# Optimization experiments

Measured on AMD Instinct MI355X. Metric: run time of the kernel, lower is better.

Reference implementation:

```python
import jax, jax.numpy as jnp
import numpy as np
import math

B, H, N, D = 4, 16, 2048, 64
EPS = 1e-8


def setup_inputs() -> dict:
    key = jax.random.key(0)
    kq, kk, kv = jax.random.split(key, 3)
    Q = jax.random.normal(kq, (B, H, N, D), dtype=jnp.float32)
    K = jax.random.normal(kk, (B, H, N, D), dtype=jnp.float32)
    V = jax.random.normal(kv, (B, H, N, D), dtype=jnp.float32)
    # learnable per-head scale, init g0 = log2(N^2 - N)
    g0 = math.log2(N * N - N)
    qk_scale = jnp.full((H,), g0, dtype=jnp.float32)
    # causal mask, broadcast over (B, H)
    M = jnp.tril(jnp.ones((N, N), dtype=bool))
    return {"Q": Q, "K": K, "V": V, "qk_scale": qk_scale, "M": M}


def reference(Q, K, V, qk_scale, M):
    # L2-normalize Q and K along head dim (cosine attention)
    Q_hat = Q / (jnp.sqrt(jnp.sum(Q * Q, axis=-1, keepdims=True)) + EPS)
    K_hat = K / (jnp.sqrt(jnp.sum(K * K, axis=-1, keepdims=True)) + EPS)
    g = qk_scale[None, :, None, None]  # per-head learnable temperature
    scores = jnp.einsum('bhnd,bhmd->bhnm', Q_hat * g, K_hat)
    scores = jnp.where(M, scores, -jnp.inf)
    attn = jax.nn.softmax(scores, axis=-1)  # stable max-subtract softmax
    return jnp.einsum('bhnm,bhmd->bhnd', attn, V)
```

## Files before the change

### kernel.cpp

```cpp
#include <hip/hip_runtime.h>


#define BATCH 4
#define HEADS 16
#define SEQ   2048
#define DIM   64
#define EPS   1e-8f
#define LOG2E 1.44269504088896340736f

typedef short bf16x8 __attribute__((ext_vector_type(8)));
typedef short s16x4  __attribute__((ext_vector_type(4)));
typedef float fx16   __attribute__((ext_vector_type(16)));
typedef unsigned int u32x4 __attribute__((ext_vector_type(4)));

static __device__ __forceinline__ short f2bf(float x) {
    unsigned u = __float_as_uint(x);
    unsigned r = (u + 0x7fffu + ((u >> 16) & 1u)) >> 16;
    return (short)r;
}
static __device__ __forceinline__ unsigned cvt_pk(float lo, float hi) {
    unsigned r;
    asm("v_cvt_pk_bf16_f32 %0, %1, %2" : "=v"(r) : "v"(lo), "v"(hi));
    return r;
}
static __device__ __forceinline__ void gload_lds16(const short* g, short* l) {
    __builtin_amdgcn_global_load_lds(
        (const __attribute__((address_space(1))) void*)g,
        (__attribute__((address_space(3))) void*)l, 16, 0, 0);
}

__global__ __launch_bounds__(256) void norm_k(
    const float* __restrict__ K, short* __restrict__ Kn)
{
    const int tid  = threadIdx.x;
    const int lane = tid & 63;
    long long rid = (long long)blockIdx.x * 16 + (tid >> 6) * 4 + (lane >> 4);
    const int c4 = (lane & 15) * 4;

    const float* src = K + rid * DIM;
    float4 v = *(const float4*)(src + c4);
    float ss = v.x * v.x + v.y * v.y + v.z * v.z + v.w * v.w;
    ss += __shfl_xor(ss, 1);
    ss += __shfl_xor(ss, 2);
    ss += __shfl_xor(ss, 4);
    ss += __shfl_xor(ss, 8);
    float s = 1.0f / (sqrtf(ss) + EPS);

    const int bh = (int)(rid >> 11);
    const int n  = (int)(rid & 2047);
    const int kt = n >> 6;
    const int r  = n & 63;
    short* dst = Kn + ((size_t)bh << 17) + (kt << 12) + (r << 6);

    s16x4 o;
    o[0] = f2bf(v.x * s);
    o[1] = f2bf(v.y * s);
    o[2] = f2bf(v.z * s);
    o[3] = f2bf(v.w * s);
    *(s16x4*)(dst + (c4 ^ ((r & 7) << 3))) = o;
}

#define TLDS 68

__global__ __launch_bounds__(256) void transpose_v(
    const float* __restrict__ V, short* __restrict__ Vt)
{
    const int nt = blockIdx.x;
    const int bh = blockIdx.y;
    const float* Vb = V + ((size_t)bh * SEQ + (size_t)nt * 64) * DIM;
    short* Vo = Vt + ((size_t)bh << 17) + (nt << 12);

    __shared__ short lds[DIM * TLDS];
    const int t  = threadIdx.x;
    const int cg = t & 15;
    const int rr = t >> 4;

#pragma unroll
    for (int i = 0; i < 4; ++i) {
        int n  = rr + i * 16;
        int d0 = cg * 4;
        float4 v = *(const float4*)(Vb + (size_t)n * DIM + d0);
        lds[(d0 + 0) * TLDS + n] = f2bf(v.x);
        lds[(d0 + 1) * TLDS + n] = f2bf(v.y);
        lds[(d0 + 2) * TLDS + n] = f2bf(v.z);
        lds[(d0 + 3) * TLDS + n] = f2bf(v.w);
    }
    __syncthreads();
#pragma unroll
    for (int i = 0; i < 4; ++i) {
        int d  = rr + i * 16;
        int nl = cg * 4;
        s16x4 o;
        o[0] = lds[d * TLDS + nl + 0];
        o[1] = lds[d * TLDS + nl + 1];
        o[2] = lds[d * TLDS + nl + 2];
        o[3] = lds[d * TLDS + nl + 3];
        *(s16x4*)(Vo + (d << 6) + (nl ^ ((d & 7) << 3))) = o;
    }
}

__global__ __launch_bounds__(128) void attn_fwd(
    const float* __restrict__ Q, const float* __restrict__ scale,
    const short* __restrict__ Kn, const short* __restrict__ Vt,
    float* __restrict__ out)
{
    const int lid = blockIdx.x;
    const int bh  = (lid & 7) * 8 + ((lid >> 3) & 7);
    const int qt  = 31 - (lid >> 6);
    const int tid = threadIdx.x;
    const int w   = tid >> 6;
    const int l   = tid & 63;
    const int lq  = l & 31;
    const int hi  = l >> 5;

    const int wlo  = qt * 64 + w * 32;
    const int qrow = wlo + lq;

    const short* Kb = Kn + ((size_t)bh << 17);
    const short* Vb = Vt + ((size_t)bh << 17);

    __shared__ __align__(16) short ldsK[2][64 * 64];
    __shared__ __align__(16) short ldsV[2][64 * 64];

    const int toff = tid * 8;

#pragma unroll
    for (int s = 0; s < 4; ++s) {
        gload_lds16(Kb + s * 1024 + toff, &ldsK[0][s * 1024 + toff]);
        gload_lds16(Vb + s * 1024 + toff, &ldsV[0][s * 1024 + toff]);
    }

    const float* Qrow = Q + ((size_t)bh * SEQ + qrow) * DIM;
    float qv[4][8];
    float ss = 0.f;
#pragma unroll
    for (int c = 0; c < 4; ++c) {
        float4 a = *(const float4*)(Qrow + c * 16 + hi * 8);
        float4 b = *(const float4*)(Qrow + c * 16 + hi * 8 + 4);
        qv[c][0] = a.x; qv[c][1] = a.y; qv[c][2] = a.z; qv[c][3] = a.w;
        qv[c][4] = b.x; qv[c][5] = b.y; qv[c][6] = b.z; qv[c][7] = b.w;
#pragma unroll
        for (int jj = 0; jj < 8; ++jj) ss += qv[c][jj] * qv[c][jj];
    }
    ss += __shfl_xor(ss, 32);
    const float g  = scale[bh & (HEADS - 1)];
    const float sc = g * LOG2E / (sqrtf(ss) + EPS);

    bf16x8 qb[4];
#pragma unroll
    for (int c = 0; c < 4; ++c) {
        u32x4 wds;
#pragma unroll
        for (int m = 0; m < 4; ++m)
            wds[m] = cvt_pk(qv[c][2 * m] * sc, qv[c][2 * m + 1] * sc);
        qb[c] = __builtin_bit_cast(bf16x8, wds);
    }

    fx16 oacc[2];
#pragma unroll
    for (int dt = 0; dt < 2; ++dt)
#pragma unroll
        for (int r = 0; r < 16; ++r) oacc[dt][r] = 0.f;
    float lsum = 0.f;

    const int nkt = qt + 1;
    int cur = 0;

    for (int kt = 0; kt < nkt; ++kt) {
        __syncthreads();

        if (kt + 1 < nkt) {
            const int nb = cur ^ 1;
            const short* gK = Kb + (size_t)(kt + 1) * 4096;
            const short* gV = Vb + (size_t)(kt + 1) * 4096;
#pragma unroll
            for (int s = 0; s < 4; ++s) {
                gload_lds16(gK + s * 1024 + toff, &ldsK[nb][s * 1024 + toff]);
                gload_lds16(gV + s * 1024 + toff, &ldsV[nb][s * 1024 + toff]);
            }
        }

        const int k0 = kt * 64;
        const short* lk = ldsK[cur];
        const short* lv = ldsV[cur];

        fx16 sacc[2];
#pragma unroll
        for (int t = 0; t < 2; ++t)
#pragma unroll
            for (int r = 0; r < 16; ++r) sacc[t][r] = 0.f;

        bf16x8 kf[2][4];
#pragma unroll
        for (int t = 0; t < 2; ++t)
#pragma unroll
            for (int c = 0; c < 4; ++c) {
                int r = t * 32 + lq;
                kf[t][c] = *(const bf16x8*)
                    &lk[(r << 6) + ((c * 16 + hi * 8) ^ ((r & 7) << 3))];
            }
        __builtin_amdgcn_s_setprio(1);
#pragma unroll
        for (int c = 0; c < 4; ++c) {
            sacc[0] = __builtin_amdgcn_mfma_f32_32x32x16_bf16(kf[0][c], qb[c], sacc[0], 0, 0, 0);
            sacc[1] = __builtin_amdgcn_mfma_f32_32x32x16_bf16(kf[1][c], qb[c], sacc[1], 0, 0, 0);
        }
        __builtin_amdgcn_s_setprio(0);

        bf16x8 vf[2][4];
#pragma unroll
        for (int dt = 0; dt < 2; ++dt)
#pragma unroll
            for (int ks = 0; ks < 4; ++ks) {
                int d = dt * 32 + lq;
                vf[dt][ks] = *(const bf16x8*)
                    &lv[(d << 6) + ((ks * 16 + hi * 8) ^ ((d & 7) << 3))];
            }

        float p[32];
#pragma unroll
        for (int t = 0; t < 2; ++t)
#pragma unroll
            for (int r = 0; r < 16; ++r) p[t * 16 + r] = sacc[t][r];

        if (kt == qt) {
#pragma unroll
            for (int t = 0; t < 2; ++t)
#pragma unroll
                for (int r = 0; r < 16; ++r) {
                    int key = k0 + 32 * t + (r & 3) + 8 * (r >> 2) + 4 * hi;
                    if (key > qrow) p[t * 16 + r] = -3.0e38f;
                }
        }

#pragma unroll
        for (int r = 0; r < 32; ++r)
            p[r] = __builtin_amdgcn_exp2f(p[r]);

        float ts[16];
#pragma unroll
        for (int r = 0; r < 16; ++r) ts[r] = p[r] + p[r + 16];
#pragma unroll
        for (int r = 0; r < 8; ++r) ts[r] += ts[r + 8];
#pragma unroll
        for (int r = 0; r < 4; ++r) ts[r] += ts[r + 4];
        float ps = (ts[0] + ts[1]) + (ts[2] + ts[3]);
        ps += __shfl_xor(ps, 32);
        lsum += ps;

        u32x4 paw[4];
#pragma unroll
        for (int ks = 0; ks < 4; ++ks) {
            const int t = ks >> 1;
            const int b0 = (ks & 1) * 8;
#pragma unroll
            for (int m = 0; m < 2; ++m) {
                unsigned a = cvt_pk(p[t * 16 + b0 + 2 * m], p[t * 16 + b0 + 2 * m + 1]);
                unsigned b = cvt_pk(p[t * 16 + b0 + 2 * m + 4], p[t * 16 + b0 + 2 * m + 5]);
                asm("v_permlane32_swap_b32 %0, %1" : "+v"(a), "+v"(b));
                paw[ks][m]     = a;
                paw[ks][m + 2] = b;
            }
        }

        __builtin_amdgcn_s_setprio(1);
#pragma unroll
        for (int dt = 0; dt < 2; ++dt)
#pragma unroll
            for (int ks = 0; ks < 4; ++ks) {
                bf16x8 pa = __builtin_bit_cast(bf16x8, paw[ks]);
                oacc[dt] = __builtin_amdgcn_mfma_f32_32x32x16_bf16(vf[dt][ks], pa, oacc[dt], 0, 0, 0);
            }
        __builtin_amdgcn_s_setprio(0);

        cur ^= 1;
    }

    float inv = 1.0f / lsum;
    size_t rb = ((size_t)bh * SEQ + (size_t)qrow) * DIM;
#pragma unroll
    for (int dt = 0; dt < 2; ++dt)
#pragma unroll
        for (int g4 = 0; g4 < 4; ++g4) {
            float4 o4;
            o4.x = oacc[dt][4 * g4 + 0] * inv;
            o4.y = oacc[dt][4 * g4 + 1] * inv;
            o4.z = oacc[dt][4 * g4 + 2] * inv;
            o4.w = oacc[dt][4 * g4 + 3] * inv;
            *(float4*)(out + rb + dt * 32 + 8 * g4 + 4 * hi) = o4;
        }
}

extern "C" void kernel_launch(void* const* d_in, const int* in_sizes, int n_in,
                              void* d_out, int out_size, void* d_ws, size_t ws_size,
                              hipStream_t stream)
{
    const float* Q  = (const float*)d_in[0];
    const float* K  = (const float*)d_in[1];
    const float* V  = (const float*)d_in[2];
    const float* qs = (const float*)d_in[3];
    float* out = (float*)d_out;

    const size_t nElem = (size_t)BATCH * HEADS * SEQ * DIM;
    short* Kn = (short*)d_ws;
    short* Vt = Kn + nElem;

    {
        long long rows = (long long)BATCH * HEADS * SEQ;
        norm_k<<<(int)(rows / 16), 256, 0, stream>>>(K, Kn);
    }
    {
        dim3 grid(SEQ / 64, BATCH * HEADS);
        transpose_v<<<grid, 256, 0, stream>>>(V, Vt);
    }
    {
        attn_fwd<<<(SEQ / 64) * BATCH * HEADS, 128, 0, stream>>>(Q, qs, Kn, Vt, out);
    }
}
```

Baseline: 86.43 us.

## Use 512-thread blocks over 256-row query tiles with paired causal phases

The attention kernel now runs 8-wave blocks, each covering a 256-row query tile, so one K/V tile load into LDS is shared by 8 waves instead of 2. Each block handles two query tiles (7-p and p) in two phases to even out causal work, with a per-wave skip of key tiles beyond its rows. The aim is to cut global-to-LDS traffic and balance load across blocks. The cost is a grid of only 256 blocks. Waves that skip tiles still wait at every barrier, and larger blocks may lower occupancy.

```diff
diff --git a/kernel.cpp b/kernel.cpp
--- a/kernel.cpp
+++ b/kernel.cpp
@@ -99,196 +99,197 @@
     }
 }
 
-__global__ __launch_bounds__(128) void attn_fwd(
+__global__ __launch_bounds__(512) void attn_fwd(
     const float* __restrict__ Q, const float* __restrict__ scale,
     const short* __restrict__ Kn, const short* __restrict__ Vt,
     float* __restrict__ out)
 {
     const int lid = blockIdx.x;
     const int bh  = (lid & 7) * 8 + ((lid >> 3) & 7);
-    const int qt  = 31 - (lid >> 6);
+    const int p   = lid >> 6;
     const int tid = threadIdx.x;
     const int w   = tid >> 6;
     const int l   = tid & 63;
     const int lq  = l & 31;
     const int hi  = l >> 5;
 
-    const int wlo  = qt * 64 + w * 32;
-    const int qrow = wlo + lq;
-
     const short* Kb = Kn + ((size_t)bh << 17);
     const short* Vb = Vt + ((size_t)bh << 17);
+    const float  g  = scale[bh & (HEADS - 1)];
 
     __shared__ __align__(16) short ldsK[2][64 * 64];
     __shared__ __align__(16) short ldsV[2][64 * 64];
 
     const int toff = tid * 8;
 
-#pragma unroll
-    for (int s = 0; s < 4; ++s) {
-        gload_lds16(Kb + s * 1024 + toff, &ldsK[0][s * 1024 + toff]);
-        gload_lds16(Vb + s * 1024 + toff, &ldsV[0][s * 1024 + toff]);
-    }
-
-    const float* Qrow = Q + ((size_t)bh * SEQ + qrow) * DIM;
-    float qv[4][8];
-    float ss = 0.f;
-#pragma unroll
-    for (int c = 0; c < 4; ++c) {
-        float4 a = *(const float4*)(Qrow + c * 16 + hi * 8);
-        float4 b = *(const float4*)(Qrow + c * 16 + hi * 8 + 4);
-        qv[c][0] = a.x; qv[c][1] = a.y; qv[c][2] = a.z; qv[c][3] = a.w;
-        qv[c][4] = b.x; qv[c][5] = b.y; qv[c][6] = b.z; qv[c][7] = b.w;
-#pragma unroll
-        for (int jj = 0; jj < 8; ++jj) ss += qv[c][jj] * qv[c][jj];
-    }
-    ss += __shfl_xor(ss, 32);
-    const float g  = scale[bh & (HEADS - 1)];
-    const float sc = g * LOG2E / (sqrtf(ss) + EPS);
-
-    bf16x8 qb[4];
-#pragma unroll
-    for (int c = 0; c < 4; ++c) {
-        u32x4 wds;
-#pragma unroll
-        for (int m = 0; m < 4; ++m)
-            wds[m] = cvt_pk(qv[c][2 * m] * sc, qv[c][2 * m + 1] * sc);
-        qb[c] = __builtin_bit_cast(bf16x8, wds);
-    }
-
-    fx16 oacc[2];
-#pragma unroll
-    for (int dt = 0; dt < 2; ++dt)
-#pragma unroll
-        for (int r = 0; r < 16; ++r) oacc[dt][r] = 0.f;
-    float lsum = 0.f;
-
-    const int nkt = qt + 1;
-    int cur = 0;
-
-    for (int kt = 0; kt < nkt; ++kt) {
+#pragma unroll 1
+    for (int phase = 0; phase < 2; ++phase) {
+        const int qb   = phase == 0 ? (7 - p) : p;
+        const int wlo  = qb * 256 + w * 32;
+        const int whi  = wlo + 31;
+        const int qrow = wlo + lq;
+        const int nkt  = 4 * qb + 4;
+
         __syncthreads();
 
-        if (kt + 1 < nkt) {
-            const int nb = cur ^ 1;
-            const short* gK = Kb + (size_t)(kt + 1) * 4096;
-            const short* gV = Vb + (size_t)(kt + 1) * 4096;
-#pragma unroll
-            for (int s = 0; s < 4; ++s) {
-                gload_lds16(gK + s * 1024 + toff, &ldsK[nb][s * 1024 + toff]);
-                gload_lds16(gV + s * 1024 + toff, &ldsV[nb][s * 1024 + toff]);
+        gload_lds16(Kb + toff, &ldsK[0][toff]);
+        gload_lds16(Vb + toff, &ldsV[0][toff]);
+
+        const float* Qrow = Q + ((size_t)bh * SEQ + qrow) * DIM;
+        float qv[4][8];
+        float ss = 0.f;
+#pragma unroll
+        for (int c = 0; c < 4; ++c) {
+            float4 a = *(const float4*)(Qrow + c * 16 + hi * 8);
+            float4 b = *(const float4*)(Qrow + c * 16 + hi * 8 + 4);
+            qv[c][0] = a.x; qv[c][1] = a.y; qv[c][2] = a.z; qv[c][3] = a.w;
+            qv[c][4] = b.x; qv[c][5] = b.y; qv[c][6] = b.z; qv[c][7] = b.w;
+#pragma unroll
+            for (int jj = 0; jj < 8; ++jj) ss += qv[c][jj] * qv[c][jj];
+        }
+        ss += __shfl_xor(ss, 32);
+        const float sc = g * LOG2E / (sqrtf(ss) + EPS);
+
+        bf16x8 qbf[4];
+#pragma unroll
+        for (int c = 0; c < 4; ++c) {
+            u32x4 wds;
+#pragma unroll
+            for (int m = 0; m < 4; ++m)
+                wds[m] = cvt_pk(qv[c][2 * m] * sc, qv[c][2 * m + 1] * sc);
+            qbf[c] = __builtin_bit_cast(bf16x8, wds);
+        }
+
+        fx16 oacc[2];
+#pragma unroll
+        for (int dt = 0; dt < 2; ++dt)
+#pragma unroll
+            for (int r = 0; r < 16; ++r) oacc[dt][r] = 0.f;
+        float lsum = 0.f;
+
+        int cur = 0;
+        for (int kt = 0; kt < nkt; ++kt) {
+            __syncthreads();
+
+            if (kt + 1 < nkt) {
+                const int nb = cur ^ 1;
+                const short* gK = Kb + (size_t)(kt + 1) * 4096;
+                const short* gV = Vb + (size_t)(kt + 1) * 4096;
+                gload_lds16(gK + toff, &ldsK[nb][toff]);
+                gload_lds16(gV + toff, &ldsV[nb][toff]);
             }
+
+            const int k0 = kt * 64;
+            if (k0 <= whi) {
+                const short* lk = ldsK[cur];
+                const short* lv = ldsV[cur];
+
+                fx16 sacc[2];
+#pragma unroll
+                for (int t = 0; t < 2; ++t)
+#pragma unroll
+                    for (int r = 0; r < 16; ++r) sacc[t][r] = 0.f;
+
+                bf16x8 kf[2][4];
+#pragma unroll
+                for (int t = 0; t < 2; ++t)
+#pragma unroll
+                    for (int c = 0; c < 4; ++c) {
+                        int r = t * 32 + lq;
+                        kf[t][c] = *(const bf16x8*)
+                            &lk[(r << 6) + ((c * 16 + hi * 8) ^ ((r & 7) << 3))];
+                    }
+                __builtin_amdgcn_s_setprio(1);
+#pragma unroll
+                for (int c = 0; c < 4; ++c) {
+                    sacc[0] = __builtin_amdgcn_mfma_f32_32x32x16_bf16(kf[0][c], qbf[c], sacc[0], 0, 0, 0);
+                    sacc[1] = __builtin_amdgcn_mfma_f32_32x32x16_bf16(kf[1][c], qbf[c], sacc[1], 0, 0, 0);
+                }
+                __builtin_amdgcn_s_setprio(0);
+
+                bf16x8 vf[2][4];
+#pragma unroll
+                for (int dt = 0; dt < 2; ++dt)
+#pragma unroll
+                    for (int ks = 0; ks < 4; ++ks) {
+                        int d = dt * 32 + lq;
+                        vf[dt][ks] = *(const bf16x8*)
+                            &lv[(d << 6) + ((ks * 16 + hi * 8) ^ ((d & 7) << 3))];
+                    }
+
+                float pv[32];
+#pragma unroll
+                for (int t = 0; t < 2; ++t)
+#pragma unroll
+                    for (int r = 0; r < 16; ++r) pv[t * 16 + r] = sacc[t][r];
+
+                if (k0 + 63 > wlo) {
+#pragma unroll
+                    for (int t = 0; t < 2; ++t)
+#pragma unroll
+                        for (int r = 0; r < 16; ++r) {
+                            int key = k0 + 32 * t + (r & 3) + 8 * (r >> 2) + 4 * hi;
+                            if (key > qrow) pv[t * 16 + r] = -3.0e38f;
+                        }
+                }
+
+#pragma unroll
+                for (int r = 0; r < 32; ++r)
+                    pv[r] = __builtin_amdgcn_exp2f(pv[r]);
+
+                float ts[16];
+#pragma unroll
+                for (int r = 0; r < 16; ++r) ts[r] = pv[r] + pv[r + 16];
+#pragma unroll
+                for (int r = 0; r < 8; ++r) ts[r] += ts[r + 8];
+#pragma unroll
+                for (int r = 0; r < 4; ++r) ts[r] += ts[r + 4];
+                float ps = (ts[0] + ts[1]) + (ts[2] + ts[3]);
+                ps += __shfl_xor(ps, 32);
+                lsum += ps;
+
+                u32x4 paw[4];
+#pragma unroll
+                for (int ks = 0; ks < 4; ++ks) {
+                    const int t = ks >> 1;
+                    const int b0 = (ks & 1) * 8;
+#pragma unroll
+                    for (int m = 0; m < 2; ++m) {
+                        unsigned a = cvt_pk(pv[t * 16 + b0 + 2 * m], pv[t * 16 + b0 + 2 * m + 1]);
+                        unsigned b = cvt_pk(pv[t * 16 + b0 + 2 * m + 4], pv[t * 16 + b0 + 2 * m + 5]);
+                        asm("v_permlane32_swap_b32 %0, %1" : "+v"(a), "+v"(b));
+                        paw[ks][m]     = a;
+                        paw[ks][m + 2] = b;
+                    }
+                }
+
+                __builtin_amdgcn_s_setprio(1);
+#pragma unroll
+                for (int dt = 0; dt < 2; ++dt)
+#pragma unroll
+                    for (int ks = 0; ks < 4; ++ks) {
+                        bf16x8 pa = __builtin_bit_cast(bf16x8, paw[ks]);
+                        oacc[dt] = __builtin_amdgcn_mfma_f32_32x32x16_bf16(vf[dt][ks], pa, oacc[dt], 0, 0, 0);
+                    }
+                __builtin_amdgcn_s_setprio(0);
+            }
+            cur ^= 1;
         }
 
-        const int k0 = kt * 64;
-        const short* lk = ldsK[cur];
-        const short* lv = ldsV[cur];
-
-        fx16 sacc[2];
-#pragma unroll
-        for (int t = 0; t < 2; ++t)
-#pragma unroll
-            for (int r = 0; r < 16; ++r) sacc[t][r] = 0.f;
-
-        bf16x8 kf[2][4];
-#pragma unroll
-        for (int t = 0; t < 2; ++t)
-#pragma unroll
-            for (int c = 0; c < 4; ++c) {
-                int r = t * 32 + lq;
-                kf[t][c] = *(const bf16x8*)
-                    &lk[(r << 6) + ((c * 16 + hi * 8) ^ ((r & 7) << 3))];
+        float inv = 1.0f / lsum;
+        size_t rb = ((size_t)bh * SEQ + (size_t)qrow) * DIM;
+#pragma unroll
+        for (int dt = 0; dt < 2; ++dt)
+#pragma unroll
+            for (int g4 = 0; g4 < 4; ++g4) {
+                float4 o4;
+                o4.x = oacc[dt][4 * g4 + 0] * inv;
+                o4.y = oacc[dt][4 * g4 + 1] * inv;
+                o4.z = oacc[dt][4 * g4 + 2] * inv;
+                o4.w = oacc[dt][4 * g4 + 3] * inv;
+                *(float4*)(out + rb + dt * 32 + 8 * g4 + 4 * hi) = o4;
             }
-        __builtin_amdgcn_s_setprio(1);
-#pragma unroll
-        for (int c = 0; c < 4; ++c) {
-            sacc[0] = __builtin_amdgcn_mfma_f32_32x32x16_bf16(kf[0][c], qb[c], sacc[0], 0, 0, 0);
-            sacc[1] = __builtin_amdgcn_mfma_f32_32x32x16_bf16(kf[1][c], qb[c], sacc[1], 0, 0, 0);
-        }
-        __builtin_amdgcn_s_setprio(0);
-
-        bf16x8 vf[2][4];
-#pragma unroll
-        for (int dt = 0; dt < 2; ++dt)
-#pragma unroll
-            for (int ks = 0; ks < 4; ++ks) {
-                int d = dt * 32 + lq;
-                vf[dt][ks] = *(const bf16x8*)
-                    &lv[(d << 6) + ((ks * 16 + hi * 8) ^ ((d & 7) << 3))];
-            }
-
-        float p[32];
-#pragma unroll
-        for (int t = 0; t < 2; ++t)
-#pragma unroll
-            for (int r = 0; r < 16; ++r) p[t * 16 + r] = sacc[t][r];
-
-        if (kt == qt) {
-#pragma unroll
-            for (int t = 0; t < 2; ++t)
-#pragma unroll
-                for (int r = 0; r < 16; ++r) {
-                    int key = k0 + 32 * t + (r & 3) + 8 * (r >> 2) + 4 * hi;
-                    if (key > qrow) p[t * 16 + r] = -3.0e38f;
-                }
-        }
-
-#pragma unroll
-        for (int r = 0; r < 32; ++r)
-            p[r] = __builtin_amdgcn_exp2f(p[r]);
-
-        float ts[16];
-#pragma unroll
-        for (int r = 0; r < 16; ++r) ts[r] = p[r] + p[r + 16];
-#pragma unroll
-        for (int r = 0; r < 8; ++r) ts[r] += ts[r + 8];
-#pragma unroll
-        for (int r = 0; r < 4; ++r) ts[r] += ts[r + 4];
-        float ps = (ts[0] + ts[1]) + (ts[2] + ts[3]);
-        ps += __shfl_xor(ps, 32);
-        lsum += ps;
-
-        u32x4 paw[4];
-#pragma unroll
-        for (int ks = 0; ks < 4; ++ks) {
-            const int t = ks >> 1;
-            const int b0 = (ks & 1) * 8;
-#pragma unroll
-            for (int m = 0; m < 2; ++m) {
-                unsigned a = cvt_pk(p[t * 16 + b0 + 2 * m], p[t * 16 + b0 + 2 * m + 1]);
-                unsigned b = cvt_pk(p[t * 16 + b0 + 2 * m + 4], p[t * 16 + b0 + 2 * m + 5]);
-                asm("v_permlane32_swap_b32 %0, %1" : "+v"(a), "+v"(b));
-                paw[ks][m]     = a;
-                paw[ks][m + 2] = b;
-            }
-        }
-
-        __builtin_amdgcn_s_setprio(1);
-#pragma unroll
-        for (int dt = 0; dt < 2; ++dt)
-#pragma unroll
-            for (int ks = 0; ks < 4; ++ks) {
-                bf16x8 pa = __builtin_bit_cast(bf16x8, paw[ks]);
-                oacc[dt] = __builtin_amdgcn_mfma_f32_32x32x16_bf16(vf[dt][ks], pa, oacc[dt], 0, 0, 0);
-            }
-        __builtin_amdgcn_s_setprio(0);
-
-        cur ^= 1;
-    }
-
-    float inv = 1.0f / lsum;
-    size_t rb = ((size_t)bh * SEQ + (size_t)qrow) * DIM;
-#pragma unroll
-    for (int dt = 0; dt < 2; ++dt)
-#pragma unroll
-        for (int g4 = 0; g4 < 4; ++g4) {
-            float4 o4;
-            o4.x = oacc[dt][4 * g4 + 0] * inv;
-            o4.y = oacc[dt][4 * g4 + 1] * inv;
-            o4.z = oacc[dt][4 * g4 + 2] * inv;
-            o4.w = oacc[dt][4 * g4 + 3] * inv;
-            *(float4*)(out + rb + dt * 32 + 8 * g4 + 4 * hi) = o4;
-        }
+    }
 }
 
 extern "C" void kernel_launch(void* const* d_in, const int* in_sizes, int n_in,
@@ -314,6 +315,6 @@
         transpose_v<<<grid, 256, 0, stream>>>(V, Vt);
     }
     {
-        attn_fwd<<<(SEQ / 64) * BATCH * HEADS, 128, 0, stream>>>(Q, qs, Kn, Vt, out);
-    }
-}
+        attn_fwd<<<(SEQ / 256 / 2) * BATCH * HEADS, 512, 0, stream>>>(Q, qs, Kn, Vt, out);
+    }
+}
```

Result: faster. 78.85 us (-8.8%).
